# Performance work log

Hardware: AMD Instinct MI355X
Metric: run time of the kernel (lower is better)

Reference implementation:

```python
import jax, jax.numpy as jnp
import numpy as np

N_NODES = 50000
N_EDGES = 400000


def _gcn_norm(edge_index, num_nodes):
    """Add self-loops and compute symmetric GCN normalization coefficients.

    Returns (src, dst, norm) where out[dst] += norm * h[src].
    """
    loop = jnp.arange(num_nodes, dtype=edge_index.dtype)
    src = jnp.concatenate([edge_index[0], loop])
    dst = jnp.concatenate([edge_index[1], loop])
    ones = jnp.ones(src.shape[0], dtype=jnp.float32)
    deg = jax.ops.segment_sum(ones, dst, num_segments=num_nodes)
    d_inv_sqrt = jnp.where(deg > 0, jax.lax.rsqrt(jnp.maximum(deg, 1.0)), 0.0)
    norm = d_inv_sqrt[src] * d_inv_sqrt[dst]
    return src, dst, norm


def _gcn_conv(x, W, b, src, dst, norm, num_nodes):
    h = x @ W                              # [N, out] dense GEMM first (PyG GCNConv order)
    msg = h[src] * norm[:, None]           # [E+N, out] gather + scale
    agg = jax.ops.segment_sum(msg, dst, num_segments=num_nodes)  # scatter-add
    return agg + b


def setup_inputs() -> dict:
    key = jax.random.key(0)
    k1, k2, k3, k4, k5, k6 = jax.random.split(key, 6)
    x = jax.random.normal(k1, (N_NODES, 128), dtype=jnp.float32)
    edge_index = jax.random.randint(k2, (2, N_EDGES), 0, N_NODES, dtype=jnp.int64)
    # Glorot-ish scaled params
    W1 = jax.random.normal(k3, (128, 512), dtype=jnp.float32) * (1.0 / np.sqrt(128))
    b1 = jnp.zeros((512,), dtype=jnp.float32)
    W2 = jax.random.normal(k4, (512, 250), dtype=jnp.float32) * (1.0 / np.sqrt(512))
    b2 = jnp.zeros((250,), dtype=jnp.float32)
    return {"x": x, "edge_index": edge_index, "W1": W1, "b1": b1, "W2": W2, "b2": b2}


def reference(x, edge_index, W1, b1, W2, b2):
    num_nodes = x.shape[0]
    src, dst, norm = _gcn_norm(edge_index, num_nodes)
    h = _gcn_conv(x, W1, b1, src, dst, norm, num_nodes)
    h = jax.nn.relu(h)
    h = _gcn_conv(h, W2, b2, src, dst, norm, num_nodes)
    return jax.nn.relu(h)
```

## Files before the change

### kernel.cpp

```cpp
#include <hip/hip_runtime.h>

constexpr int NN  = 50000;
constexpr int NE  = 400000;
constexpr int F0  = 128;
constexpr int F1  = 512;
constexpr int F2  = 250;
constexpr int MT64 = 782;
constexpr int SLOT = 64;

typedef short  short8 __attribute__((ext_vector_type(8)));
typedef float  f32x4  __attribute__((ext_vector_type(4)));

__device__ inline unsigned short f2bf(float f) {
    union { float f; unsigned u; } v; v.f = f;
    unsigned u = v.u;
    return (unsigned short)((u + 0x7FFFu + ((u >> 16) & 1u)) >> 16);
}
__device__ inline float bf2f(unsigned short h) {
    union { unsigned u; float f; } v; v.u = ((unsigned)h) << 16;
    return v.f;
}
__device__ inline float bflo(unsigned u) {
    union { unsigned u; float f; } v; v.u = u << 16; return v.f;
}
__device__ inline float bfhi(unsigned u) {
    union { unsigned u; float f; } v; v.u = u & 0xFFFF0000u; return v.f;
}

__global__ void k_build(const int4* __restrict__ src4, const int4* __restrict__ dst4,
                        int* __restrict__ cnt, int* __restrict__ slot) {
    int t = blockIdx.x * 256 + threadIdx.x;
    if (t >= NE / 4) return;
    int4 s = src4[t];
    int4 d = dst4[t];
    int p;
    p = atomicAdd(&cnt[d.x], 1); if (p < SLOT) slot[d.x * SLOT + p] = s.x;
    p = atomicAdd(&cnt[d.y], 1); if (p < SLOT) slot[d.y * SLOT + p] = s.y;
    p = atomicAdd(&cnt[d.z], 1); if (p < SLOT) slot[d.z * SLOT + p] = s.z;
    p = atomicAdd(&cnt[d.w], 1); if (p < SLOT) slot[d.w * SLOT + p] = s.w;
}

__global__ __launch_bounds__(256) void k_prep(
        const float4* __restrict__ x4, const int* __restrict__ cnt,
        ushort4* __restrict__ xs,
        const float* __restrict__ W1, unsigned short* __restrict__ w1t,
        const float* __restrict__ W2, unsigned short* __restrict__ w2t) {
    int b = blockIdx.x;
    if (b < 6250) {
        int t = b * 256 + threadIdx.x;
        float dn = rsqrtf((float)cnt[t >> 5] + 1.0f);
        float4 v = x4[t];
        ushort4 o;
        o.x = f2bf(dn * v.x); o.y = f2bf(dn * v.y);
        o.z = f2bf(dn * v.z); o.w = f2bf(dn * v.w);
        xs[t] = o;
    } else if (b < 6250 + 256) {
        int t = (b - 6250) * 256 + threadIdx.x;
        int n = t >> 7, k = t & 127;
        w1t[t] = f2bf(W1[k * F1 + n]);
    } else {
        int t = (b - 6506) * 256 + threadIdx.x;
        int n = t >> 9, k = t & 511;
        w2t[t] = (n < F2) ? f2bf(W2[k * F2 + n]) : (unsigned short)0;
    }
}

__global__ __launch_bounds__(256) void k_gather1(
        const unsigned int* __restrict__ xs, const int* __restrict__ slot,
        const int* __restrict__ cnt, unsigned int* __restrict__ agg) {
    int n = blockIdx.x * 4 + (threadIdx.x >> 6);
    int c = threadIdx.x & 63;
    if (n >= NN) return;
    int deg = cnt[n]; if (deg > SLOT) deg = SLOT;
    float dn = rsqrtf((float)deg + 1.0f);
    const int* sl = slot + n * SLOT;
    unsigned a = xs[(size_t)n * 64 + c];
    float s0 = bflo(a), s1 = bfhi(a);
    int j = 0;
    for (; j + 8 <= deg; j += 8) {
        int i0 = sl[j],     i1 = sl[j + 1], i2 = sl[j + 2], i3 = sl[j + 3];
        int i4 = sl[j + 4], i5 = sl[j + 5], i6 = sl[j + 6], i7 = sl[j + 7];
        unsigned v0 = xs[(size_t)i0 * 64 + c];
        unsigned v1 = xs[(size_t)i1 * 64 + c];
        unsigned v2 = xs[(size_t)i2 * 64 + c];
        unsigned v3 = xs[(size_t)i3 * 64 + c];
        unsigned v4 = xs[(size_t)i4 * 64 + c];
        unsigned v5 = xs[(size_t)i5 * 64 + c];
        unsigned v6 = xs[(size_t)i6 * 64 + c];
        unsigned v7 = xs[(size_t)i7 * 64 + c];
        s0 += bflo(v0) + bflo(v1) + bflo(v2) + bflo(v3)
            + bflo(v4) + bflo(v5) + bflo(v6) + bflo(v7);
        s1 += bfhi(v0) + bfhi(v1) + bfhi(v2) + bfhi(v3)
            + bfhi(v4) + bfhi(v5) + bfhi(v6) + bfhi(v7);
    }
    for (; j + 4 <= deg; j += 4) {
        int i0 = sl[j], i1 = sl[j + 1], i2 = sl[j + 2], i3 = sl[j + 3];
        unsigned v0 = xs[(size_t)i0 * 64 + c];
        unsigned v1 = xs[(size_t)i1 * 64 + c];
        unsigned v2 = xs[(size_t)i2 * 64 + c];
        unsigned v3 = xs[(size_t)i3 * 64 + c];
        s0 += bflo(v0) + bflo(v1) + bflo(v2) + bflo(v3);
        s1 += bfhi(v0) + bfhi(v1) + bfhi(v2) + bfhi(v3);
    }
    for (; j < deg; ++j) {
        unsigned v = xs[(size_t)sl[j] * 64 + c];
        s0 += bflo(v); s1 += bfhi(v);
    }
    agg[(size_t)n * 64 + c] =
        (unsigned)f2bf(dn * s0) | ((unsigned)f2bf(dn * s1) << 16);
}

__global__ __launch_bounds__(256) void k_fused(
        const unsigned short* __restrict__ A,
        const unsigned short* __restrict__ W1t,
        const unsigned short* __restrict__ W2t,
        const float* __restrict__ b1,
        const int* __restrict__ cnt,
        unsigned short* __restrict__ C,
        int M)
{
    __shared__ unsigned short H[64 * 512];

    const int tid = threadIdx.x;
    const int wv = tid >> 6, ln = tid & 63;
    const int lane15 = ln & 15, quad = ln >> 4;
    const int m0 = blockIdx.x * 64;

    short8 af[4][4];
#pragma unroll
    for (int rf = 0; rf < 4; ++rf) {
        int arow = m0 + rf * 16 + lane15; if (arow > M - 1) arow = M - 1;
        const short8* ap = (const short8*)(A + (size_t)arow * 128);
#pragma unroll
        for (int kk = 0; kk < 4; ++kk)
            af[rf][kk] = ap[kk * 4 + quad];
    }

#pragma unroll 2
    for (int f = 0; f < 8; ++f) {
        const int nB = wv * 128 + f * 16 + lane15;
        const short8* bp = (const short8*)(W1t + (size_t)nB * 128);
        short8 bf[4];
#pragma unroll
        for (int kk = 0; kk < 4; ++kk) bf[kk] = bp[kk * 4 + quad];
        f32x4 acc[4];
#pragma unroll
        for (int rf = 0; rf < 4; ++rf) acc[rf] = (f32x4)0.0f;
#pragma unroll
        for (int kk = 0; kk < 4; ++kk)
#pragma unroll
            for (int rf = 0; rf < 4; ++rf)
                acc[rf] = __builtin_amdgcn_mfma_f32_16x16x32_bf16(
                    af[rf][kk], bf[kk], acc[rf], 0, 0, 0);
        const float bia = b1[nB];
#pragma unroll
        for (int rf = 0; rf < 4; ++rf)
#pragma unroll
            for (int r = 0; r < 4; ++r) {
                int lrow = rf * 16 + quad * 4 + r;
                unsigned byteoff = (unsigned)(lrow * 1024 + nB * 2)
                                 ^ (unsigned)((lrow & 7) << 4);
                *(unsigned short*)((char*)H + byteoff) =
                    f2bf(fmaxf(acc[rf][r] + bia, 0.0f));
            }
    }

    __syncthreads();

    f32x4 acc2[4][4];
#pragma unroll
    for (int rf = 0; rf < 4; ++rf)
#pragma unroll
        for (int cf = 0; cf < 4; ++cf)
            acc2[rf][cf] = (f32x4)0.0f;

#pragma unroll 2
    for (int ks = 0; ks < 16; ++ks) {
        short8 bf[4];
#pragma unroll
        for (int cf = 0; cf < 4; ++cf) {
            int nB = wv * 64 + cf * 16 + lane15;
            bf[cf] = *(const short8*)(W2t + (size_t)nB * 512 + ks * 32 + quad * 8);
        }
        short8 hf[4];
#pragma unroll
        for (int rf = 0; rf < 4; ++rf) {
            int lrow = rf * 16 + lane15;
            unsigned byteoff = (unsigned)(lrow * 1024 + (ks * 32 + quad * 8) * 2)
                             ^ (unsigned)((lrow & 7) << 4);
            hf[rf] = *(const short8*)((const char*)H + byteoff);
        }
#pragma unroll
        for (int rf = 0; rf < 4; ++rf)
#pragma unroll
            for (int cf = 0; cf < 4; ++cf)
                acc2[rf][cf] = __builtin_amdgcn_mfma_f32_16x16x32_bf16(
                    hf[rf], bf[cf], acc2[rf][cf], 0, 0, 0);
    }

#pragma unroll
    for (int rf = 0; rf < 4; ++rf) {
        float rs[4];
#pragma unroll
        for (int r = 0; r < 4; ++r) {
            int row = m0 + rf * 16 + quad * 4 + r; if (row > M - 1) row = M - 1;
            rs[r] = rsqrtf((float)cnt[row] + 1.0f);
        }
#pragma unroll
        for (int cf = 0; cf < 4; ++cf) {
            int col = wv * 64 + cf * 16 + lane15;
            f32x4 v = acc2[rf][cf];
#pragma unroll
            for (int r = 0; r < 4; ++r) {
                int row = m0 + rf * 16 + quad * 4 + r;
                if (row < M)
                    C[(size_t)row * 256 + col] = f2bf(v[r] * rs[r]);
            }
        }
    }
}

__global__ __launch_bounds__(256) void k_gather2(
        const ushort4* __restrict__ t4, const int* __restrict__ slot,
        const int* __restrict__ cnt, const float* __restrict__ b2,
        float* __restrict__ out) {
    int n = blockIdx.x * 4 + (threadIdx.x >> 6);
    int c = threadIdx.x & 63;
    if (n >= NN) return;
    int deg = cnt[n]; if (deg > SLOT) deg = SLOT;
    float dn = rsqrtf((float)deg + 1.0f);
    const int* sl = slot + n * SLOT;
    ushort4 a = t4[(size_t)n * 64 + c];
    float sx = bf2f(a.x), sy = bf2f(a.y), sz = bf2f(a.z), sw = bf2f(a.w);
    int j = 0;
    for (; j + 8 <= deg; j += 8) {
        int i0 = sl[j],     i1 = sl[j + 1], i2 = sl[j + 2], i3 = sl[j + 3];
        int i4 = sl[j + 4], i5 = sl[j + 5], i6 = sl[j + 6], i7 = sl[j + 7];
        ushort4 v0 = t4[(size_t)i0 * 64 + c];
        ushort4 v1 = t4[(size_t)i1 * 64 + c];
        ushort4 v2 = t4[(size_t)i2 * 64 + c];
        ushort4 v3 = t4[(size_t)i3 * 64 + c];
        ushort4 v4 = t4[(size_t)i4 * 64 + c];
        ushort4 v5 = t4[(size_t)i5 * 64 + c];
        ushort4 v6 = t4[(size_t)i6 * 64 + c];
        ushort4 v7 = t4[(size_t)i7 * 64 + c];
        sx += bf2f(v0.x) + bf2f(v1.x) + bf2f(v2.x) + bf2f(v3.x)
            + bf2f(v4.x) + bf2f(v5.x) + bf2f(v6.x) + bf2f(v7.x);
        sy += bf2f(v0.y) + bf2f(v1.y) + bf2f(v2.y) + bf2f(v3.y)
            + bf2f(v4.y) + bf2f(v5.y) + bf2f(v6.y) + bf2f(v7.y);
        sz += bf2f(v0.z) + bf2f(v1.z) + bf2f(v2.z) + bf2f(v3.z)
            + bf2f(v4.z) + bf2f(v5.z) + bf2f(v6.z) + bf2f(v7.z);
        sw += bf2f(v0.w) + bf2f(v1.w) + bf2f(v2.w) + bf2f(v3.w)
            + bf2f(v4.w) + bf2f(v5.w) + bf2f(v6.w) + bf2f(v7.w);
    }
    for (; j + 4 <= deg; j += 4) {
        int i0 = sl[j], i1 = sl[j + 1], i2 = sl[j + 2], i3 = sl[j + 3];
        ushort4 v0 = t4[(size_t)i0 * 64 + c];
        ushort4 v1 = t4[(size_t)i1 * 64 + c];
        ushort4 v2 = t4[(size_t)i2 * 64 + c];
        ushort4 v3 = t4[(size_t)i3 * 64 + c];
        sx += bf2f(v0.x) + bf2f(v1.x) + bf2f(v2.x) + bf2f(v3.x);
        sy += bf2f(v0.y) + bf2f(v1.y) + bf2f(v2.y) + bf2f(v3.y);
        sz += bf2f(v0.z) + bf2f(v1.z) + bf2f(v2.z) + bf2f(v3.z);
        sw += bf2f(v0.w) + bf2f(v1.w) + bf2f(v2.w) + bf2f(v3.w);
    }
    for (; j < deg; ++j) {
        ushort4 v = t4[(size_t)sl[j] * 64 + c];
        sx += bf2f(v.x); sy += bf2f(v.y); sz += bf2f(v.z); sw += bf2f(v.w);
    }
    int f = c * 4;
    float* o = out + (size_t)n * F2;
    if (f     < F2) o[f]     = fmaxf(dn * sx + b2[f],     0.f);
    if (f + 1 < F2) o[f + 1] = fmaxf(dn * sy + b2[f + 1], 0.f);
    if (f + 2 < F2) o[f + 2] = fmaxf(dn * sz + b2[f + 2], 0.f);
    if (f + 3 < F2) o[f + 3] = fmaxf(dn * sw + b2[f + 3], 0.f);
}

extern "C" void kernel_launch(void* const* d_in, const int* in_sizes, int n_in,
                              void* d_out, int out_size, void* d_ws, size_t ws_size,
                              hipStream_t stream) {
    const float* x  = (const float*)d_in[0];
    const int*   ei = (const int*)d_in[1];
    const float* W1 = (const float*)d_in[2];
    const float* b1 = (const float*)d_in[3];
    const float* W2 = (const float*)d_in[4];
    const float* b2 = (const float*)d_in[5];
    float* out = (float*)d_out;

    char* p = (char*)d_ws;
    auto carve = [&](size_t bytes) { char* r = p; p += (bytes + 255) & ~(size_t)255; return r; };
    int*            cnt  = (int*)carve(NN * 4);
    int*            slot = (int*)carve((size_t)NN * SLOT * 4);
    unsigned short* xs   = (unsigned short*)carve((size_t)NN * F0 * 2);
    unsigned short* agg1 = (unsigned short*)carve((size_t)NN * F0 * 2);
    unsigned short* t2s  = (unsigned short*)carve((size_t)NN * 256 * 2);
    unsigned short* w1t  = (unsigned short*)carve((size_t)F1 * F0 * 2);
    unsigned short* w2t  = (unsigned short*)carve((size_t)256 * F1 * 2);

    hipMemsetAsync(cnt, 0, NN * sizeof(int), stream);
    k_build<<<(NE / 4 + 255) / 256, 256, 0, stream>>>(
        (const int4*)ei, (const int4*)(ei + NE), cnt, slot);
    k_prep<<<6250 + 256 + 512, 256, 0, stream>>>(
        (const float4*)x, cnt, (ushort4*)xs, W1, w1t, W2, w2t);
    k_gather1<<<(NN + 3) / 4, 256, 0, stream>>>((const unsigned int*)xs, slot, cnt,
                                                (unsigned int*)agg1);
    k_fused<<<MT64, 256, 0, stream>>>(agg1, w1t, w2t, b1, cnt, t2s, NN);
    k_gather2<<<(NN + 3) / 4, 256, 0, stream>>>((const ushort4*)t2s, slot, cnt, b2, out);
}
```

Before: 237.4 us.

## Halve fused GEMM row tile and swap MFMA operands for packed stores

The fused two-layer GEMM kernel now processes 32 rows per block instead of 64, which doubles the grid and halves shared memory per block, and it asks for 4 blocks per CU through launch bounds. The MFMA operands are swapped so that weights take the A side and activations the B side. As a result each lane holds four consecutive output columns, so the hidden tile and the output can be written as packed 8-byte stores instead of scattered 2-byte stores, and the bias loads as a vector. The cost is that each weight fragment loaded is now reused across half as many rows, which raises weight traffic from L2.

```diff
diff --git a/kernel.cpp b/kernel.cpp
--- a/kernel.cpp
+++ b/kernel.cpp
@@ -5,11 +5,12 @@
 constexpr int F0  = 128;
 constexpr int F1  = 512;
 constexpr int F2  = 250;
-constexpr int MT64 = 782;
+constexpr int MT32 = 1564;
 constexpr int SLOT = 64;
 
-typedef short  short8 __attribute__((ext_vector_type(8)));
-typedef float  f32x4  __attribute__((ext_vector_type(4)));
+typedef short    short8 __attribute__((ext_vector_type(8)));
+typedef float    f32x4  __attribute__((ext_vector_type(4)));
+typedef unsigned u32x2  __attribute__((ext_vector_type(2)));
 
 __device__ inline unsigned short f2bf(float f) {
     union { float f; unsigned u; } v; v.f = f;
@@ -110,7 +111,7 @@
         (unsigned)f2bf(dn * s0) | ((unsigned)f2bf(dn * s1) << 16);
 }
 
-__global__ __launch_bounds__(256) void k_fused(
+__global__ __launch_bounds__(256, 4) void k_fused(
         const unsigned short* __restrict__ A,
         const unsigned short* __restrict__ W1t,
         const unsigned short* __restrict__ W2t,
@@ -119,102 +120,95 @@
         unsigned short* __restrict__ C,
         int M)
 {
-    __shared__ unsigned short H[64 * 512];
+    __shared__ unsigned short H[32 * 512];
 
     const int tid = threadIdx.x;
     const int wv = tid >> 6, ln = tid & 63;
     const int lane15 = ln & 15, quad = ln >> 4;
-    const int m0 = blockIdx.x * 64;
-
-    short8 af[4][4];
-#pragma unroll
-    for (int rf = 0; rf < 4; ++rf) {
-        int arow = m0 + rf * 16 + lane15; if (arow > M - 1) arow = M - 1;
+    const int m0 = blockIdx.x * 32;
+    const unsigned hxor = (unsigned)((lane15 & 7) << 4);
+
+    short8 bfA[2][4];
+#pragma unroll
+    for (int nf = 0; nf < 2; ++nf) {
+        int arow = m0 + nf * 16 + lane15; if (arow > M - 1) arow = M - 1;
         const short8* ap = (const short8*)(A + (size_t)arow * 128);
 #pragma unroll
+        for (int kk = 0; kk < 4; ++kk) bfA[nf][kk] = ap[kk * 4 + quad];
+    }
+
+    for (int f = 0; f < 8; ++f) {
+        const int hbase = wv * 128 + f * 16;
+        const short8* wp = (const short8*)(W1t + (size_t)(hbase + lane15) * 128);
+        short8 af[4];
+#pragma unroll
+        for (int kk = 0; kk < 4; ++kk) af[kk] = wp[kk * 4 + quad];
+        f32x4 acc[2];
+        acc[0] = (f32x4)0.0f; acc[1] = (f32x4)0.0f;
+#pragma unroll
         for (int kk = 0; kk < 4; ++kk)
-            af[rf][kk] = ap[kk * 4 + quad];
-    }
-
-#pragma unroll 2
-    for (int f = 0; f < 8; ++f) {
-        const int nB = wv * 128 + f * 16 + lane15;
-        const short8* bp = (const short8*)(W1t + (size_t)nB * 128);
-        short8 bf[4];
-#pragma unroll
-        for (int kk = 0; kk < 4; ++kk) bf[kk] = bp[kk * 4 + quad];
-        f32x4 acc[4];
-#pragma unroll
-        for (int rf = 0; rf < 4; ++rf) acc[rf] = (f32x4)0.0f;
-#pragma unroll
-        for (int kk = 0; kk < 4; ++kk)
-#pragma unroll
-            for (int rf = 0; rf < 4; ++rf)
-                acc[rf] = __builtin_amdgcn_mfma_f32_16x16x32_bf16(
-                    af[rf][kk], bf[kk], acc[rf], 0, 0, 0);
-        const float bia = b1[nB];
-#pragma unroll
-        for (int rf = 0; rf < 4; ++rf)
-#pragma unroll
-            for (int r = 0; r < 4; ++r) {
-                int lrow = rf * 16 + quad * 4 + r;
-                unsigned byteoff = (unsigned)(lrow * 1024 + nB * 2)
-                                 ^ (unsigned)((lrow & 7) << 4);
-                *(unsigned short*)((char*)H + byteoff) =
-                    f2bf(fmaxf(acc[rf][r] + bia, 0.0f));
-            }
+#pragma unroll
+            for (int nf = 0; nf < 2; ++nf)
+                acc[nf] = __builtin_amdgcn_mfma_f32_16x16x32_bf16(
+                    af[kk], bfA[nf][kk], acc[nf], 0, 0, 0);
+        f32x4 bias4 = *(const f32x4*)(b1 + hbase + quad * 4);
+#pragma unroll
+        for (int nf = 0; nf < 2; ++nf) {
+            u32x2 o;
+            o.x = (unsigned)f2bf(fmaxf(acc[nf][0] + bias4[0], 0.0f))
+                | ((unsigned)f2bf(fmaxf(acc[nf][1] + bias4[1], 0.0f)) << 16);
+            o.y = (unsigned)f2bf(fmaxf(acc[nf][2] + bias4[2], 0.0f))
+                | ((unsigned)f2bf(fmaxf(acc[nf][3] + bias4[3], 0.0f)) << 16);
+            unsigned off = (unsigned)((nf * 16 + lane15) * 1024
+                                      + hbase * 2 + quad * 8) ^ hxor;
+            *(u32x2*)((char*)H + off) = o;
+        }
     }
 
     __syncthreads();
 
-    f32x4 acc2[4][4];
-#pragma unroll
-    for (int rf = 0; rf < 4; ++rf)
-#pragma unroll
-        for (int cf = 0; cf < 4; ++cf)
-            acc2[rf][cf] = (f32x4)0.0f;
+    f32x4 acc2[4][2];
+#pragma unroll
+    for (int cf = 0; cf < 4; ++cf)
+#pragma unroll
+        for (int nf = 0; nf < 2; ++nf)
+            acc2[cf][nf] = (f32x4)0.0f;
 
 #pragma unroll 2
     for (int ks = 0; ks < 16; ++ks) {
-        short8 bf[4];
-#pragma unroll
-        for (int cf = 0; cf < 4; ++cf) {
-            int nB = wv * 64 + cf * 16 + lane15;
-            bf[cf] = *(const short8*)(W2t + (size_t)nB * 512 + ks * 32 + quad * 8);
+        short8 af2[4];
+#pragma unroll
+        for (int cf = 0; cf < 4; ++cf)
+            af2[cf] = *(const short8*)(W2t
+                + (size_t)(wv * 64 + cf * 16 + lane15) * 512 + ks * 32 + quad * 8);
+        short8 bf2[2];
+#pragma unroll
+        for (int nf = 0; nf < 2; ++nf) {
+            unsigned off = (unsigned)((nf * 16 + lane15) * 1024
+                                      + ks * 64 + quad * 16) ^ hxor;
+            bf2[nf] = *(const short8*)((const char*)H + off);
         }
-        short8 hf[4];
-#pragma unroll
-        for (int rf = 0; rf < 4; ++rf) {
-            int lrow = rf * 16 + lane15;
-            unsigned byteoff = (unsigned)(lrow * 1024 + (ks * 32 + quad * 8) * 2)
-                             ^ (unsigned)((lrow & 7) << 4);
-            hf[rf] = *(const short8*)((const char*)H + byteoff);
-        }
-#pragma unroll
-        for (int rf = 0; rf < 4; ++rf)
-#pragma unroll
-            for (int cf = 0; cf < 4; ++cf)
-                acc2[rf][cf] = __builtin_amdgcn_mfma_f32_16x16x32_bf16(
-                    hf[rf], bf[cf], acc2[rf][cf], 0, 0, 0);
-    }
-
-#pragma unroll
-    for (int rf = 0; rf < 4; ++rf) {
-        float rs[4];
-#pragma unroll
-        for (int r = 0; r < 4; ++r) {
-            int row = m0 + rf * 16 + quad * 4 + r; if (row > M - 1) row = M - 1;
-            rs[r] = rsqrtf((float)cnt[row] + 1.0f);
-        }
-#pragma unroll
-        for (int cf = 0; cf < 4; ++cf) {
-            int col = wv * 64 + cf * 16 + lane15;
-            f32x4 v = acc2[rf][cf];
-#pragma unroll
-            for (int r = 0; r < 4; ++r) {
-                int row = m0 + rf * 16 + quad * 4 + r;
-                if (row < M)
-                    C[(size_t)row * 256 + col] = f2bf(v[r] * rs[r]);
+#pragma unroll
+        for (int cf = 0; cf < 4; ++cf)
+#pragma unroll
+            for (int nf = 0; nf < 2; ++nf)
+                acc2[cf][nf] = __builtin_amdgcn_mfma_f32_16x16x32_bf16(
+                    af2[cf], bf2[nf], acc2[cf][nf], 0, 0, 0);
+    }
+
+#pragma unroll
+    for (int nf = 0; nf < 2; ++nf) {
+        int row = m0 + nf * 16 + lane15;
+        if (row < M) {
+            float rs = rsqrtf((float)cnt[row] + 1.0f);
+#pragma unroll
+            for (int cf = 0; cf < 4; ++cf) {
+                f32x4 v = acc2[cf][nf];
+                u32x2 o;
+                o.x = (unsigned)f2bf(v[0] * rs) | ((unsigned)f2bf(v[1] * rs) << 16);
+                o.y = (unsigned)f2bf(v[2] * rs) | ((unsigned)f2bf(v[3] * rs) << 16);
+                int col = wv * 64 + cf * 16 + quad * 4;
+                *(u32x2*)(C + (size_t)row * 256 + col) = o;
             }
         }
     }
@@ -304,6 +298,6 @@
         (const float4*)x, cnt, (ushort4*)xs, W1, w1t, W2, w2t);
     k_gather1<<<(NN + 3) / 4, 256, 0, stream>>>((const unsigned int*)xs, slot, cnt,
                                                 (unsigned int*)agg1);
-    k_fused<<<MT64, 256, 0, stream>>>(agg1, w1t, w2t, b1, cnt, t2s, NN);
+    k_fused<<<MT32, 256, 0, stream>>>(agg1, w1t, w2t, b1, cnt, t2s, NN);
     k_gather2<<<(NN + 3) / 4, 256, 0, stream>>>((const ushort4*)t2s, slot, cnt, b2, out);
 }
```

Result: slower. 263.2 us (+10.8%).
